# Kernel optimization log

Measured on AMD Instinct MI355X. Metric: run time of the kernel, lower is better.

## Reference

```python
import jax, jax.numpy as jnp
import numpy as np

B, C, G, K, S, P, R = 4, 256, 16, 7, 1, 3, 4
H = W = 56


def setup_inputs() -> dict:
    key = jax.random.key(0)
    k1, k2, k3 = jax.random.split(key, 3)
    x = jax.random.normal(k1, (B, C, H, W), jnp.float32)
    reduce_w = jax.random.normal(k2, (C // R, C), jnp.float32) * 0.05
    reduce_b = jnp.zeros((C // R,), jnp.float32)
    span_w = jax.random.normal(k3, (K * K * G, C // R), jnp.float32) * 0.05
    span_b = jnp.zeros((K * K * G,), jnp.float32)
    return {"x": x, "reduce_w": reduce_w, "reduce_b": reduce_b,
            "span_w": span_w, "span_b": span_b}


def reference(x, reduce_w, reduce_b, span_w, span_b):
    b, c, h_in, w_in = x.shape
    Ho = (h_in + 2 * P - K) // S + 1
    Wo = (w_in + 2 * P - K) // S + 1
    # im2col patches, channel ordering (C, kh, kw) — matches torch.nn.Unfold
    patches = jax.lax.conv_general_dilated_patches(
        x, (K, K), (S, S), [(P, P), (P, P)])  # (B, C*K*K, Ho, Wo)
    patches = patches.reshape(b, G, c // G, K * K, Ho, Wo)
    # kernel generation branch: AvgPool(s) (identity for s=1) -> 1x1 reduce -> 1x1 span
    if S > 1:
        xk = jax.lax.reduce_window(x, 0.0, jax.lax.add,
                                   (1, 1, S, S), (1, 1, S, S), 'VALID') / (S * S)
    else:
        xk = x
    h = jnp.einsum('bchw,oc->bohw', xk, reduce_w) + reduce_b[None, :, None, None]
    kern = jnp.einsum('bchw,oc->bohw', h, span_w) + span_b[None, :, None, None]
    kern = kern.reshape(b, G, 1, K * K, Ho, Wo)
    # dynamic per-pixel depthwise-style multiply-reduce over the K*K window
    out = (kern * patches).sum(axis=3)  # (B, G, C//G, Ho, Wo)
    return out.reshape(b, c, Ho, Wo)
```

## Files before the change

kernel.cpp:

```cpp
#include <hip/hip_runtime.h>
#include <hip/hip_fp16.h>
#include <stdint.h>

#define HH   56
#define WW   56
#define HWP  3136
#define CC   256
#define GG   16
#define CGR  16
#define KT   7
#define KK   49
#define RCP  32
#define TH   2
#define XROW 32
#define XPL  260

typedef _Float16 h2_t  __attribute__((ext_vector_type(2)));
typedef __fp16   fp16x2 __attribute__((ext_vector_type(2)));
typedef _Float16 v8h  __attribute__((ext_vector_type(8)));
typedef float    v4f  __attribute__((ext_vector_type(4)));
union pk32 { uint32_t u; h2_t h; __half2 hh; fp16x2 f; };
union frag { uint32_t u[4]; v8h h; };

static __device__ __forceinline__ uint32_t pkrtz(float a, float b) {
    pk32 p; p.f = __builtin_amdgcn_cvt_pkrtz(a, b); return p.u;
}

__global__ __launch_bounds__(256)
void pack_weights(const float* __restrict__ sw, const float* __restrict__ rw,
                  uint32_t* __restrict__ sw2, uint32_t* __restrict__ rw2)
{
    const int id = blockIdx.x * 256 + threadIdx.x;
    if (id < 25088) sw2[id] = pkrtz(sw[2 * id], sw[2 * id + 1]);
    else            rw2[id - 25088] = pkrtz(rw[2 * (id - 25088)], rw[2 * (id - 25088) + 1]);
}

__global__ __launch_bounds__(256)
void gemm1_mfma(const uint32_t* __restrict__ rw2, const float* __restrict__ rb,
                const float* __restrict__ x, uint32_t* __restrict__ h2)
{
    const int b = blockIdx.z, px0 = blockIdx.x * 32;
    const int t = threadIdx.x;
    const int wave = t >> 6, lane = t & 63, quad = lane >> 4, n16 = lane & 15;

    __shared__ __align__(16) uint32_t ldsB[2][8 * 128];

    const int px = t & 31;
    const int q4 = t >> 5;
    const float* xb = x + (size_t)b * CC * HWP + px0 + px;

    float r[4][8];
#pragma unroll
    for (int k = 0; k < 4; ++k)
#pragma unroll
        for (int cc = 0; cc < 8; ++cc)
            r[k][cc] = xb[(size_t)(k * 64 + q4 * 8 + cc) * HWP];

    {
        uint4 w;
        w.x = pkrtz(r[0][0], r[0][1]); w.y = pkrtz(r[0][2], r[0][3]);
        w.z = pkrtz(r[0][4], r[0][5]); w.w = pkrtz(r[0][6], r[0][7]);
        *(uint4*)&ldsB[0][q4 * 128 + px * 4] = w;
    }
    __syncthreads();

    v4f acc[2];
    acc[0] = v4f{0.f,0.f,0.f,0.f}; acc[1] = v4f{0.f,0.f,0.f,0.f};
    const uint32_t* rwm = rw2 + (size_t)(wave * 16 + n16) * 128;
#pragma unroll
    for (int k = 0; k < 4; ++k) {
        if (k < 3) {
            uint4 w;
            w.x = pkrtz(r[k+1][0], r[k+1][1]); w.y = pkrtz(r[k+1][2], r[k+1][3]);
            w.z = pkrtz(r[k+1][4], r[k+1][5]); w.w = pkrtz(r[k+1][6], r[k+1][7]);
            *(uint4*)&ldsB[(k + 1) & 1][q4 * 128 + px * 4] = w;
        }
        frag a0, a1;
        *(uint4*)a0.u = *(const uint4*)&rwm[k * 32 + quad * 4];
        *(uint4*)a1.u = *(const uint4*)&rwm[k * 32 + 16 + quad * 4];
        const uint32_t* B = ldsB[k & 1];
#pragma unroll
        for (int nt = 0; nt < 2; ++nt) {
            frag b0, b1;
            *(uint4*)b0.u = *(const uint4*)&B[quad * 128 + (nt * 16 + n16) * 4];
            *(uint4*)b1.u = *(const uint4*)&B[(4 + quad) * 128 + (nt * 16 + n16) * 4];
            acc[nt] = __builtin_amdgcn_mfma_f32_16x16x32_f16(a0.h, b0.h, acc[nt], 0, 0, 0);
            acc[nt] = __builtin_amdgcn_mfma_f32_16x16x32_f16(a1.h, b1.h, acc[nt], 0, 0, 0);
        }
        __syncthreads();
    }
    uint32_t* hb = h2 + (size_t)b * RCP * HWP + px0;
#pragma unroll
    for (int nt = 0; nt < 2; ++nt)
#pragma unroll
        for (int pr = 0; pr < 2; ++pr) {
            const int m0 = wave * 16 + quad * 4 + 2 * pr;
            hb[(size_t)(wave * 8 + quad * 2 + pr) * HWP + nt * 16 + n16] =
                pkrtz(acc[nt][2 * pr] + rb[m0], acc[nt][2 * pr + 1] + rb[m0 + 1]);
        }
}

__global__ __launch_bounds__(256, 4)
void invol_fused(const float* __restrict__ x, const uint32_t* __restrict__ h2,
                 const uint32_t* __restrict__ sw2, const float* __restrict__ sb,
                 float* __restrict__ out)
{
    const int h0 = blockIdx.x * TH, g = blockIdx.y, b = blockIdx.z;

    __shared__ __align__(16) uint32_t sXh[16 * XPL];
    __shared__ __align__(16) uint32_t U[8 * 448];

    const int t = threadIdx.x;
    const int wave = t >> 6, lane = t & 63, quad = lane >> 4, n16 = lane & 15;

    const int mt0 = wave * 16 + n16;
    const int mtap = mt0 > 48 ? 48 : mt0;
    const uint32_t* swr = sw2 + ((size_t)g * KK + mtap) * RCP + quad * 4;
    frag a0, a1;
    *(uint4*)a0.u = *(const uint4*)swr;
    *(uint4*)a1.u = *(const uint4*)(swr + 16);

    float bvv[4];
#pragma unroll
    for (int reg = 0; reg < 4; ++reg) {
        const int tp = wave * 16 + quad * 4 + reg;
        bvv[reg] = (tp < KK) ? sb[g * KK + tp] : 0.f;
    }

    {
        const uint32_t* hb = h2 + (size_t)b * RCP * HWP + h0 * WW;
#pragma unroll
        for (int k = 0; k < 4; ++k) {
            const int i = t + 256 * k;
            if (i < 896) {
                const int px = i % 112, q4 = i / 112;
                uint4 w;
                w.x = hb[(size_t)(q4 * 4 + 0) * HWP + px];
                w.y = hb[(size_t)(q4 * 4 + 1) * HWP + px];
                w.z = hb[(size_t)(q4 * 4 + 2) * HWP + px];
                w.w = hb[(size_t)(q4 * 4 + 3) * HWP + px];
                *(uint4*)&U[q4 * 448 + px * 4] = w;
            }
        }
    }

    {
        const int ch = t >> 4, rr = (t >> 1) & 7, side = t & 1;
        uint2 z; z.x = 0; z.y = 0;
        *(uint2*)&sXh[ch * XPL + rr * XROW + (side ? 30 : 0)] = z;
    }

    {
        const float* xb = x + (size_t)(b * CC + g * CGR) * HWP;
#pragma unroll
        for (int k = 0; k < 7; ++k) {
            const int i = t + 256 * k;
            const int w4 = i % 14, rr = (i / 14) % 8, ch = i / 112;
            const int hh = h0 - 3 + rr;
            float4 v = make_float4(0.f, 0.f, 0.f, 0.f);
            if (hh >= 0 && hh < HH)
                v = *(const float4*)&xb[(size_t)ch * HWP + hh * WW + 4 * w4];
            uint2 p; p.x = pkrtz(v.x, v.y); p.y = pkrtz(v.z, v.w);
            *(uint2*)&sXh[ch * XPL + rr * XROW + 2 + 2 * w4] = p;
        }
    }
    __syncthreads();

    v4f acc[7];
#pragma unroll
    for (int nt = 0; nt < 7; ++nt) acc[nt] = v4f{0.f,0.f,0.f,0.f};
#pragma unroll
    for (int nt = 0; nt < 7; ++nt) {
        const int pxm = (nt * 16 + n16) * 4;
        frag b0, b1;
        *(uint4*)b0.u = *(const uint4*)&U[quad * 448 + pxm];
        *(uint4*)b1.u = *(const uint4*)&U[(4 + quad) * 448 + pxm];
        acc[nt] = __builtin_amdgcn_mfma_f32_16x16x32_f16(a0.h, b0.h, acc[nt], 0, 0, 0);
        acc[nt] = __builtin_amdgcn_mfma_f32_16x16x32_f16(a1.h, b1.h, acc[nt], 0, 0, 0);
    }
    __syncthreads();

    {
        _Float16* sK = (_Float16*)U;
#pragma unroll
        for (int nt = 0; nt < 7; ++nt) {
            const int px = nt * 16 + n16;
#pragma unroll
            for (int reg = 0; reg < 4; ++reg) {
                const int tp = wave * 16 + quad * 4 + reg;
                if (tp < KK) sK[tp * 112 + px] = (_Float16)(acc[nt][reg] + bvv[reg]);
            }
        }
    }
    __syncthreads();

    if (t < 224) {
        const int ch = t & 15, q = t >> 4, r = q & 1, wq = q >> 1;
        const uint32_t* xpl = &sXh[ch * XPL + 4 * wq];
        float o0=0,o1=0,o2=0,o3=0,o4=0,o5=0,o6=0,o7=0;
#pragma unroll
        for (int kh = 0; kh < KT; ++kh) {
            const int rr = r + kh;
            uint32_t E[8];
            *(uint4*)&E[0] = *(const uint4*)&xpl[rr * XROW];
            *(uint4*)&E[4] = *(const uint4*)&xpl[rr * XROW + 4];
            uint32_t O[7];
#pragma unroll
            for (int j = 0; j < 7; ++j) O[j] = __builtin_amdgcn_alignbit(E[j + 1], E[j], 16);
            pk32 va0, va1, va2, va3;
            va0.u = va1.u = va2.u = va3.u = 0;
            const uint32_t* kq = &U[(kh * KT) * 56 + r * 28 + 4 * wq];
#pragma unroll
            for (int kw = 0; kw < KT; ++kw) {
                const uint4 kk = *(const uint4*)&kq[kw * 56];
                pk32 k0, k1, k2, k3; k0.u = kk.x; k1.u = kk.y; k2.u = kk.z; k3.u = kk.w;
                pk32 s0, s1, s2, s3;
                if (kw & 1) {
                    const int e = (kw + 1) >> 1;
                    s0.u = E[e]; s1.u = E[e + 1]; s2.u = E[e + 2]; s3.u = E[e + 3];
                } else {
                    const int oI = kw >> 1;
                    s0.u = O[oI]; s1.u = O[oI + 1]; s2.u = O[oI + 2]; s3.u = O[oI + 3];
                }
                va0.hh = __hfma2(k0.hh, s0.hh, va0.hh);
                va1.hh = __hfma2(k1.hh, s1.hh, va1.hh);
                va2.hh = __hfma2(k2.hh, s2.hh, va2.hh);
                va3.hh = __hfma2(k3.hh, s3.hh, va3.hh);
            }
            const float2 f0 = __half22float2(va0.hh); o0 += f0.x; o1 += f0.y;
            const float2 f1 = __half22float2(va1.hh); o2 += f1.x; o3 += f1.y;
            const float2 f2 = __half22float2(va2.hh); o4 += f2.x; o5 += f2.y;
            const float2 f3 = __half22float2(va3.hh); o6 += f3.x; o7 += f3.y;
        }
        float* op = out + (size_t)(b * CC + g * CGR + ch) * HWP + (h0 + r) * WW + 8 * wq;
        *(float4*)&op[0] = make_float4(o0, o1, o2, o3);
        *(float4*)&op[4] = make_float4(o4, o5, o6, o7);
    }
}

extern "C" void kernel_launch(void* const* d_in, const int* in_sizes, int n_in,
                              void* d_out, int out_size, void* d_ws, size_t ws_size,
                              hipStream_t stream)
{
    const float* x  = (const float*)d_in[0];
    const float* rw = (const float*)d_in[1];
    const float* rb = (const float*)d_in[2];
    const float* sw = (const float*)d_in[3];
    const float* sb = (const float*)d_in[4];
    float* out  = (float*)d_out;

    uint32_t* h2  = (uint32_t*)d_ws;
    uint32_t* sw2 = h2 + 4 * RCP * HWP;
    uint32_t* rw2 = sw2 + 25088;

    pack_weights<<<dim3(130, 1, 1), 256, 0, stream>>>(sw, rw, sw2, rw2);
    gemm1_mfma<<<dim3(HWP / 32, 1, 4), 256, 0, stream>>>(rw2, rb, x, h2);
    invol_fused<<<dim3(HH / TH, GG, 4), 256, 0, stream>>>(x, h2, sw2, sb, out);
}
```

Measured before the change: 96.14 us.

## Drop weight-pack kernel, enlarge involution row tile, two channels per thread

Removes the separate pack_weights launch; both GEMM kernels now read fp32 weights and convert them to fp16 fragments inline. The first GEMM halves its pixel tile to 16 so it launches more blocks. The involution kernel doubles its row tile to 4 rows (more MFMA tiles, larger LDS, fewer halo rows per output) and each thread now handles two channels so the kernel-weight LDS loads are reused. In exchange, LDS use and registers per block go up and occupancy drops to 3 blocks per unit, and the involution grid shrinks by half.

```diff
diff --git a/kernel.cpp b/kernel.cpp
--- a/kernel.cpp
+++ b/kernel.cpp
@@ -11,14 +11,16 @@
 #define KT   7
 #define KK   49
 #define RCP  32
-#define TH   2
-#define XROW 32
-#define XPL  260
-
-typedef _Float16 h2_t  __attribute__((ext_vector_type(2)));
+#define TH   4
+#define NPX  (TH * WW)
+#define XROW 36
+#define XPL  364
+#define BQ4  (NPX * 4)
+
+typedef _Float16 h2_t   __attribute__((ext_vector_type(2)));
 typedef __fp16   fp16x2 __attribute__((ext_vector_type(2)));
-typedef _Float16 v8h  __attribute__((ext_vector_type(8)));
-typedef float    v4f  __attribute__((ext_vector_type(4)));
+typedef _Float16 v8h    __attribute__((ext_vector_type(8)));
+typedef float    v4f    __attribute__((ext_vector_type(4)));
 union pk32 { uint32_t u; h2_t h; __half2 hh; fp16x2 f; };
 union frag { uint32_t u[4]; v8h h; };
 
@@ -26,99 +28,86 @@
     pk32 p; p.f = __builtin_amdgcn_cvt_pkrtz(a, b); return p.u;
 }
 
+static __device__ __forceinline__ frag pack_afrag(const float* rowp, int quad) {
+    frag a;
+    const float4 p0 = *(const float4*)&rowp[quad * 8];
+    const float4 p1 = *(const float4*)&rowp[quad * 8 + 4];
+    a.u[0] = pkrtz(p0.x, p0.y); a.u[1] = pkrtz(p0.z, p0.w);
+    a.u[2] = pkrtz(p1.x, p1.y); a.u[3] = pkrtz(p1.z, p1.w);
+    return a;
+}
+
 __global__ __launch_bounds__(256)
-void pack_weights(const float* __restrict__ sw, const float* __restrict__ rw,
-                  uint32_t* __restrict__ sw2, uint32_t* __restrict__ rw2)
-{
-    const int id = blockIdx.x * 256 + threadIdx.x;
-    if (id < 25088) sw2[id] = pkrtz(sw[2 * id], sw[2 * id + 1]);
-    else            rw2[id - 25088] = pkrtz(rw[2 * (id - 25088)], rw[2 * (id - 25088) + 1]);
-}
-
-__global__ __launch_bounds__(256)
-void gemm1_mfma(const uint32_t* __restrict__ rw2, const float* __restrict__ rb,
+void gemm1_mfma(const float* __restrict__ rw, const float* __restrict__ rb,
                 const float* __restrict__ x, uint32_t* __restrict__ h2)
 {
-    const int b = blockIdx.z, px0 = blockIdx.x * 32;
+    const int b = blockIdx.z, px0 = blockIdx.x * 16;
     const int t = threadIdx.x;
     const int wave = t >> 6, lane = t & 63, quad = lane >> 4, n16 = lane & 15;
 
-    __shared__ __align__(16) uint32_t ldsB[2][8 * 128];
-
-    const int px = t & 31;
-    const int q4 = t >> 5;
+    __shared__ __align__(16) uint32_t ldsB[2][512];
+
+    const int px = t & 15;
+    const int cp = t >> 4;
     const float* xb = x + (size_t)b * CC * HWP + px0 + px;
 
-    float r[4][8];
-#pragma unroll
-    for (int k = 0; k < 4; ++k)
-#pragma unroll
-        for (int cc = 0; cc < 8; ++cc)
-            r[k][cc] = xb[(size_t)(k * 64 + q4 * 8 + cc) * HWP];
-
-    {
-        uint4 w;
-        w.x = pkrtz(r[0][0], r[0][1]); w.y = pkrtz(r[0][2], r[0][3]);
-        w.z = pkrtz(r[0][4], r[0][5]); w.w = pkrtz(r[0][6], r[0][7]);
-        *(uint4*)&ldsB[0][q4 * 128 + px * 4] = w;
-    }
-    __syncthreads();
-
-    v4f acc[2];
-    acc[0] = v4f{0.f,0.f,0.f,0.f}; acc[1] = v4f{0.f,0.f,0.f,0.f};
-    const uint32_t* rwm = rw2 + (size_t)(wave * 16 + n16) * 128;
+    float ra[4][4];
+#pragma unroll
+    for (int k = 0; k < 4; ++k) {
+        ra[k][0] = xb[(size_t)(k * 64 + 2 * cp) * HWP];
+        ra[k][1] = xb[(size_t)(k * 64 + 2 * cp + 1) * HWP];
+        ra[k][2] = xb[(size_t)(k * 64 + 2 * cp + 32) * HWP];
+        ra[k][3] = xb[(size_t)(k * 64 + 2 * cp + 33) * HWP];
+    }
+    const int q4a = cp >> 2, jja = cp & 3;
+    ldsB[0][q4a * 64 + px * 4 + jja]       = pkrtz(ra[0][0], ra[0][1]);
+    ldsB[0][(q4a + 4) * 64 + px * 4 + jja] = pkrtz(ra[0][2], ra[0][3]);
+    __syncthreads();
+
+    const float* rwr = rw + (size_t)(wave * 16 + n16) * CC;
+    v4f acc = v4f{0.f, 0.f, 0.f, 0.f};
 #pragma unroll
     for (int k = 0; k < 4; ++k) {
         if (k < 3) {
-            uint4 w;
-            w.x = pkrtz(r[k+1][0], r[k+1][1]); w.y = pkrtz(r[k+1][2], r[k+1][3]);
-            w.z = pkrtz(r[k+1][4], r[k+1][5]); w.w = pkrtz(r[k+1][6], r[k+1][7]);
-            *(uint4*)&ldsB[(k + 1) & 1][q4 * 128 + px * 4] = w;
-        }
-        frag a0, a1;
-        *(uint4*)a0.u = *(const uint4*)&rwm[k * 32 + quad * 4];
-        *(uint4*)a1.u = *(const uint4*)&rwm[k * 32 + 16 + quad * 4];
-        const uint32_t* B = ldsB[k & 1];
-#pragma unroll
-        for (int nt = 0; nt < 2; ++nt) {
-            frag b0, b1;
-            *(uint4*)b0.u = *(const uint4*)&B[quad * 128 + (nt * 16 + n16) * 4];
-            *(uint4*)b1.u = *(const uint4*)&B[(4 + quad) * 128 + (nt * 16 + n16) * 4];
-            acc[nt] = __builtin_amdgcn_mfma_f32_16x16x32_f16(a0.h, b0.h, acc[nt], 0, 0, 0);
-            acc[nt] = __builtin_amdgcn_mfma_f32_16x16x32_f16(a1.h, b1.h, acc[nt], 0, 0, 0);
-        }
-        __syncthreads();
+            ldsB[(k + 1) & 1][q4a * 64 + px * 4 + jja]       = pkrtz(ra[k+1][0], ra[k+1][1]);
+            ldsB[(k + 1) & 1][(q4a + 4) * 64 + px * 4 + jja] = pkrtz(ra[k+1][2], ra[k+1][3]);
+        }
+        const frag a0 = pack_afrag(rwr + k * 64, quad);
+        const frag a1 = pack_afrag(rwr + k * 64 + 32, quad);
+        frag b0, b1;
+        *(uint4*)b0.u = *(const uint4*)&ldsB[k & 1][quad * 64 + n16 * 4];
+        *(uint4*)b1.u = *(const uint4*)&ldsB[k & 1][(4 + quad) * 64 + n16 * 4];
+        acc = __builtin_amdgcn_mfma_f32_16x16x32_f16(a0.h, b0.h, acc, 0, 0, 0);
+        acc = __builtin_amdgcn_mfma_f32_16x16x32_f16(a1.h, b1.h, acc, 0, 0, 0);
+        if (k < 3) __syncthreads();
     }
     uint32_t* hb = h2 + (size_t)b * RCP * HWP + px0;
 #pragma unroll
-    for (int nt = 0; nt < 2; ++nt)
-#pragma unroll
-        for (int pr = 0; pr < 2; ++pr) {
-            const int m0 = wave * 16 + quad * 4 + 2 * pr;
-            hb[(size_t)(wave * 8 + quad * 2 + pr) * HWP + nt * 16 + n16] =
-                pkrtz(acc[nt][2 * pr] + rb[m0], acc[nt][2 * pr + 1] + rb[m0 + 1]);
-        }
-}
-
-__global__ __launch_bounds__(256, 4)
+    for (int pr = 0; pr < 2; ++pr) {
+        const int m0 = wave * 16 + quad * 4 + 2 * pr;
+        hb[(size_t)(wave * 8 + quad * 2 + pr) * HWP + n16] =
+            pkrtz(acc[2 * pr] + rb[m0], acc[2 * pr + 1] + rb[m0 + 1]);
+    }
+}
+
+__global__ __launch_bounds__(256, 3)
 void invol_fused(const float* __restrict__ x, const uint32_t* __restrict__ h2,
-                 const uint32_t* __restrict__ sw2, const float* __restrict__ sb,
+                 const float* __restrict__ sw, const float* __restrict__ sb,
                  float* __restrict__ out)
 {
     const int h0 = blockIdx.x * TH, g = blockIdx.y, b = blockIdx.z;
 
     __shared__ __align__(16) uint32_t sXh[16 * XPL];
-    __shared__ __align__(16) uint32_t U[8 * 448];
+    __shared__ __align__(16) uint32_t U[8 * BQ4];
 
     const int t = threadIdx.x;
     const int wave = t >> 6, lane = t & 63, quad = lane >> 4, n16 = lane & 15;
 
     const int mt0 = wave * 16 + n16;
     const int mtap = mt0 > 48 ? 48 : mt0;
-    const uint32_t* swr = sw2 + ((size_t)g * KK + mtap) * RCP + quad * 4;
-    frag a0, a1;
-    *(uint4*)a0.u = *(const uint4*)swr;
-    *(uint4*)a1.u = *(const uint4*)(swr + 16);
+    const float* swr = sw + (size_t)(g * KK + mtap) * 64;
+    const frag a0 = pack_afrag(swr, quad);
+    const frag a1 = pack_afrag(swr + 32, quad);
 
     float bvv[4];
 #pragma unroll
@@ -130,51 +119,55 @@
     {
         const uint32_t* hb = h2 + (size_t)b * RCP * HWP + h0 * WW;
 #pragma unroll
-        for (int k = 0; k < 4; ++k) {
+        for (int k = 0; k < 7; ++k) {
             const int i = t + 256 * k;
-            if (i < 896) {
-                const int px = i % 112, q4 = i / 112;
-                uint4 w;
-                w.x = hb[(size_t)(q4 * 4 + 0) * HWP + px];
-                w.y = hb[(size_t)(q4 * 4 + 1) * HWP + px];
-                w.z = hb[(size_t)(q4 * 4 + 2) * HWP + px];
-                w.w = hb[(size_t)(q4 * 4 + 3) * HWP + px];
-                *(uint4*)&U[q4 * 448 + px * 4] = w;
-            }
-        }
-    }
-
-    {
-        const int ch = t >> 4, rr = (t >> 1) & 7, side = t & 1;
-        uint2 z; z.x = 0; z.y = 0;
-        *(uint2*)&sXh[ch * XPL + rr * XROW + (side ? 30 : 0)] = z;
+            const int px = i % NPX, q4 = i / NPX;
+            uint4 w;
+            w.x = hb[(size_t)(q4 * 4 + 0) * HWP + px];
+            w.y = hb[(size_t)(q4 * 4 + 1) * HWP + px];
+            w.z = hb[(size_t)(q4 * 4 + 2) * HWP + px];
+            w.w = hb[(size_t)(q4 * 4 + 3) * HWP + px];
+            *(uint4*)&U[q4 * BQ4 + px * 4] = w;
+        }
+    }
+
+#pragma unroll
+    for (int k = 0; k < 2; ++k) {
+        const int i = t + 256 * k;
+        if (i < 320) {
+            const int ch = i / 20, rem = i % 20, rr = rem >> 1, side = rem & 1;
+            uint2 z; z.x = 0; z.y = 0;
+            *(uint2*)&sXh[ch * XPL + rr * XROW + (side ? 30 : 0)] = z;
+        }
     }
 
     {
         const float* xb = x + (size_t)(b * CC + g * CGR) * HWP;
 #pragma unroll
-        for (int k = 0; k < 7; ++k) {
+        for (int k = 0; k < 9; ++k) {
             const int i = t + 256 * k;
-            const int w4 = i % 14, rr = (i / 14) % 8, ch = i / 112;
-            const int hh = h0 - 3 + rr;
-            float4 v = make_float4(0.f, 0.f, 0.f, 0.f);
-            if (hh >= 0 && hh < HH)
-                v = *(const float4*)&xb[(size_t)ch * HWP + hh * WW + 4 * w4];
-            uint2 p; p.x = pkrtz(v.x, v.y); p.y = pkrtz(v.z, v.w);
-            *(uint2*)&sXh[ch * XPL + rr * XROW + 2 + 2 * w4] = p;
-        }
-    }
-    __syncthreads();
-
-    v4f acc[7];
-#pragma unroll
-    for (int nt = 0; nt < 7; ++nt) acc[nt] = v4f{0.f,0.f,0.f,0.f};
-#pragma unroll
-    for (int nt = 0; nt < 7; ++nt) {
+            if (i < 2240) {
+                const int w4 = i % 14, rr = (i / 14) % 10, ch = i / 140;
+                const int hh = h0 - 3 + rr;
+                float4 v = make_float4(0.f, 0.f, 0.f, 0.f);
+                if (hh >= 0 && hh < HH)
+                    v = *(const float4*)&xb[(size_t)ch * HWP + hh * WW + 4 * w4];
+                uint2 p; p.x = pkrtz(v.x, v.y); p.y = pkrtz(v.z, v.w);
+                *(uint2*)&sXh[ch * XPL + rr * XROW + 2 + 2 * w4] = p;
+            }
+        }
+    }
+    __syncthreads();
+
+    v4f acc[14];
+#pragma unroll
+    for (int nt = 0; nt < 14; ++nt) acc[nt] = v4f{0.f, 0.f, 0.f, 0.f};
+#pragma unroll
+    for (int nt = 0; nt < 14; ++nt) {
         const int pxm = (nt * 16 + n16) * 4;
         frag b0, b1;
-        *(uint4*)b0.u = *(const uint4*)&U[quad * 448 + pxm];
-        *(uint4*)b1.u = *(const uint4*)&U[(4 + quad) * 448 + pxm];
+        *(uint4*)b0.u = *(const uint4*)&U[quad * BQ4 + pxm];
+        *(uint4*)b1.u = *(const uint4*)&U[(4 + quad) * BQ4 + pxm];
         acc[nt] = __builtin_amdgcn_mfma_f32_16x16x32_f16(a0.h, b0.h, acc[nt], 0, 0, 0);
         acc[nt] = __builtin_amdgcn_mfma_f32_16x16x32_f16(a1.h, b1.h, acc[nt], 0, 0, 0);
     }
@@ -183,58 +176,91 @@
     {
         _Float16* sK = (_Float16*)U;
 #pragma unroll
-        for (int nt = 0; nt < 7; ++nt) {
+        for (int nt = 0; nt < 14; ++nt) {
             const int px = nt * 16 + n16;
 #pragma unroll
             for (int reg = 0; reg < 4; ++reg) {
                 const int tp = wave * 16 + quad * 4 + reg;
-                if (tp < KK) sK[tp * 112 + px] = (_Float16)(acc[nt][reg] + bvv[reg]);
+                if (tp < KK) sK[tp * NPX + px] = (_Float16)(acc[nt][reg] + bvv[reg]);
             }
         }
     }
     __syncthreads();
 
     if (t < 224) {
-        const int ch = t & 15, q = t >> 4, r = q & 1, wq = q >> 1;
-        const uint32_t* xpl = &sXh[ch * XPL + 4 * wq];
-        float o0=0,o1=0,o2=0,o3=0,o4=0,o5=0,o6=0,o7=0;
+        const int chq = t & 7, q = t >> 3;
+        const int r = q / 7, wq = q % 7;
+        const int ch0 = 2 * chq;
+        const uint32_t* xp0 = &sXh[ch0 * XPL + 4 * wq];
+        const uint32_t* xp1 = &sXh[(ch0 + 1) * XPL + 4 * wq];
+        float oa[2][8];
+#pragma unroll
+        for (int c = 0; c < 2; ++c)
+#pragma unroll
+            for (int j = 0; j < 8; ++j) oa[c][j] = 0.f;
+
 #pragma unroll
         for (int kh = 0; kh < KT; ++kh) {
             const int rr = r + kh;
-            uint32_t E[8];
-            *(uint4*)&E[0] = *(const uint4*)&xpl[rr * XROW];
-            *(uint4*)&E[4] = *(const uint4*)&xpl[rr * XROW + 4];
-            uint32_t O[7];
-#pragma unroll
-            for (int j = 0; j < 7; ++j) O[j] = __builtin_amdgcn_alignbit(E[j + 1], E[j], 16);
-            pk32 va0, va1, va2, va3;
-            va0.u = va1.u = va2.u = va3.u = 0;
-            const uint32_t* kq = &U[(kh * KT) * 56 + r * 28 + 4 * wq];
+            uint32_t E0[8], E1[8], O0[7], O1[7];
+            *(uint4*)&E0[0] = *(const uint4*)&xp0[rr * XROW];
+            *(uint4*)&E0[4] = *(const uint4*)&xp0[rr * XROW + 4];
+            *(uint4*)&E1[0] = *(const uint4*)&xp1[rr * XROW];
+            *(uint4*)&E1[4] = *(const uint4*)&xp1[rr * XROW + 4];
+#pragma unroll
+            for (int j = 0; j < 7; ++j) {
+                O0[j] = __builtin_amdgcn_alignbit(E0[j + 1], E0[j], 16);
+                O1[j] = __builtin_amdgcn_alignbit(E1[j + 1], E1[j], 16);
+            }
+            pk32 va[2][4];
+#pragma unroll
+            for (int c = 0; c < 2; ++c)
+#pragma unroll
+                for (int j = 0; j < 4; ++j) va[c][j].u = 0;
+
+            const uint32_t* kq = &U[(kh * KT) * (NPX / 2) + r * 28 + 4 * wq];
 #pragma unroll
             for (int kw = 0; kw < KT; ++kw) {
-                const uint4 kk = *(const uint4*)&kq[kw * 56];
+                const uint4 kk = *(const uint4*)&kq[kw * (NPX / 2)];
                 pk32 k0, k1, k2, k3; k0.u = kk.x; k1.u = kk.y; k2.u = kk.z; k3.u = kk.w;
-                pk32 s0, s1, s2, s3;
+                uint32_t s0, s1, s2, s3, u0, u1, u2, u3;
                 if (kw & 1) {
                     const int e = (kw + 1) >> 1;
-                    s0.u = E[e]; s1.u = E[e + 1]; s2.u = E[e + 2]; s3.u = E[e + 3];
+                    s0 = E0[e]; s1 = E0[e + 1]; s2 = E0[e + 2]; s3 = E0[e + 3];
+                    u0 = E1[e]; u1 = E1[e + 1]; u2 = E1[e + 2]; u3 = E1[e + 3];
                 } else {
                     const int oI = kw >> 1;
-                    s0.u = O[oI]; s1.u = O[oI + 1]; s2.u = O[oI + 2]; s3.u = O[oI + 3];
+                    s0 = O0[oI]; s1 = O0[oI + 1]; s2 = O0[oI + 2]; s3 = O0[oI + 3];
+                    u0 = O1[oI]; u1 = O1[oI + 1]; u2 = O1[oI + 2]; u3 = O1[oI + 3];
                 }
-                va0.hh = __hfma2(k0.hh, s0.hh, va0.hh);
-                va1.hh = __hfma2(k1.hh, s1.hh, va1.hh);
-                va2.hh = __hfma2(k2.hh, s2.hh, va2.hh);
-                va3.hh = __hfma2(k3.hh, s3.hh, va3.hh);
-            }
-            const float2 f0 = __half22float2(va0.hh); o0 += f0.x; o1 += f0.y;
-            const float2 f1 = __half22float2(va1.hh); o2 += f1.x; o3 += f1.y;
-            const float2 f2 = __half22float2(va2.hh); o4 += f2.x; o5 += f2.y;
-            const float2 f3 = __half22float2(va3.hh); o6 += f3.x; o7 += f3.y;
-        }
-        float* op = out + (size_t)(b * CC + g * CGR + ch) * HWP + (h0 + r) * WW + 8 * wq;
-        *(float4*)&op[0] = make_float4(o0, o1, o2, o3);
-        *(float4*)&op[4] = make_float4(o4, o5, o6, o7);
+                pk32 t0, t1, t2, t3;
+                t0.u = s0; t1.u = s1; t2.u = s2; t3.u = s3;
+                va[0][0].hh = __hfma2(k0.hh, t0.hh, va[0][0].hh);
+                va[0][1].hh = __hfma2(k1.hh, t1.hh, va[0][1].hh);
+                va[0][2].hh = __hfma2(k2.hh, t2.hh, va[0][2].hh);
+                va[0][3].hh = __hfma2(k3.hh, t3.hh, va[0][3].hh);
+                t0.u = u0; t1.u = u1; t2.u = u2; t3.u = u3;
+                va[1][0].hh = __hfma2(k0.hh, t0.hh, va[1][0].hh);
+                va[1][1].hh = __hfma2(k1.hh, t1.hh, va[1][1].hh);
+                va[1][2].hh = __hfma2(k2.hh, t2.hh, va[1][2].hh);
+                va[1][3].hh = __hfma2(k3.hh, t3.hh, va[1][3].hh);
+            }
+#pragma unroll
+            for (int c = 0; c < 2; ++c)
+#pragma unroll
+                for (int j = 0; j < 4; ++j) {
+                    const float2 f = __half22float2(va[c][j].hh);
+                    oa[c][2 * j]     += f.x;
+                    oa[c][2 * j + 1] += f.y;
+                }
+        }
+#pragma unroll
+        for (int c = 0; c < 2; ++c) {
+            float* op = out + (size_t)(b * CC + g * CGR + ch0 + c) * HWP
+                            + (h0 + r) * WW + 8 * wq;
+            *(float4*)&op[0] = make_float4(oa[c][0], oa[c][1], oa[c][2], oa[c][3]);
+            *(float4*)&op[4] = make_float4(oa[c][4], oa[c][5], oa[c][6], oa[c][7]);
+        }
     }
 }
 
@@ -249,11 +275,8 @@
     const float* sb = (const float*)d_in[4];
     float* out  = (float*)d_out;
 
-    uint32_t* h2  = (uint32_t*)d_ws;
-    uint32_t* sw2 = h2 + 4 * RCP * HWP;
-    uint32_t* rw2 = sw2 + 25088;
-
-    pack_weights<<<dim3(130, 1, 1), 256, 0, stream>>>(sw, rw, sw2, rw2);
-    gemm1_mfma<<<dim3(HWP / 32, 1, 4), 256, 0, stream>>>(rw2, rb, x, h2);
-    invol_fused<<<dim3(HH / TH, GG, 4), 256, 0, stream>>>(x, h2, sw2, sb, out);
-}
+    uint32_t* h2 = (uint32_t*)d_ws;
+
+    gemm1_mfma<<<dim3(HWP / 16, 1, 4), 256, 0, stream>>>(rw, rb, x, h2);
+    invol_fused<<<dim3(HH / TH, GG, 4), 256, 0, stream>>>(x, h2, sw, sb, out);
+}
```

Result: slower. 103.3 us (+7.4%).

## Fuse weight packing into consumer kernels and compute two channels per thread

Applied to the files above, without the earlier changes.

Removes the separate pack_weights launch: gemm1 and invol_fused now read fp32 weights directly and convert them to fp16 MFMA fragments in registers. The involution reduction stage now has 112 threads, each handling two channels, so every kernel-weight LDS load feeds twice as many FMAs. This saves one kernel launch and the round trip through the workspace. In exchange it adds redundant per-block conversion work, raises register pressure, and halves the thread parallelism of the reduction stage.

```diff
diff --git a/kernel.cpp b/kernel.cpp
--- a/kernel.cpp
+++ b/kernel.cpp
@@ -15,10 +15,10 @@
 #define XROW 32
 #define XPL  260
 
-typedef _Float16 h2_t  __attribute__((ext_vector_type(2)));
+typedef _Float16 h2_t   __attribute__((ext_vector_type(2)));
 typedef __fp16   fp16x2 __attribute__((ext_vector_type(2)));
-typedef _Float16 v8h  __attribute__((ext_vector_type(8)));
-typedef float    v4f  __attribute__((ext_vector_type(4)));
+typedef _Float16 v8h    __attribute__((ext_vector_type(8)));
+typedef float    v4f    __attribute__((ext_vector_type(4)));
 union pk32 { uint32_t u; h2_t h; __half2 hh; fp16x2 f; };
 union frag { uint32_t u[4]; v8h h; };
 
@@ -26,17 +26,17 @@
     pk32 p; p.f = __builtin_amdgcn_cvt_pkrtz(a, b); return p.u;
 }
 
+static __device__ __forceinline__ frag pack_afrag(const float* rowp, int quad) {
+    frag a;
+    const float4 p0 = *(const float4*)&rowp[quad * 8];
+    const float4 p1 = *(const float4*)&rowp[quad * 8 + 4];
+    a.u[0] = pkrtz(p0.x, p0.y); a.u[1] = pkrtz(p0.z, p0.w);
+    a.u[2] = pkrtz(p1.x, p1.y); a.u[3] = pkrtz(p1.z, p1.w);
+    return a;
+}
+
 __global__ __launch_bounds__(256)
-void pack_weights(const float* __restrict__ sw, const float* __restrict__ rw,
-                  uint32_t* __restrict__ sw2, uint32_t* __restrict__ rw2)
-{
-    const int id = blockIdx.x * 256 + threadIdx.x;
-    if (id < 25088) sw2[id] = pkrtz(sw[2 * id], sw[2 * id + 1]);
-    else            rw2[id - 25088] = pkrtz(rw[2 * (id - 25088)], rw[2 * (id - 25088) + 1]);
-}
-
-__global__ __launch_bounds__(256)
-void gemm1_mfma(const uint32_t* __restrict__ rw2, const float* __restrict__ rb,
+void gemm1_mfma(const float* __restrict__ rw, const float* __restrict__ rb,
                 const float* __restrict__ x, uint32_t* __restrict__ h2)
 {
     const int b = blockIdx.z, px0 = blockIdx.x * 32;
@@ -56,6 +56,14 @@
         for (int cc = 0; cc < 8; ++cc)
             r[k][cc] = xb[(size_t)(k * 64 + q4 * 8 + cc) * HWP];
 
+    const float* rwr = rw + (size_t)(wave * 16 + n16) * CC;
+    frag af0[4], af1[4];
+#pragma unroll
+    for (int k = 0; k < 4; ++k) {
+        af0[k] = pack_afrag(rwr + k * 64, quad);
+        af1[k] = pack_afrag(rwr + k * 64 + 32, quad);
+    }
+
     {
         uint4 w;
         w.x = pkrtz(r[0][0], r[0][1]); w.y = pkrtz(r[0][2], r[0][3]);
@@ -66,7 +74,6 @@
 
     v4f acc[2];
     acc[0] = v4f{0.f,0.f,0.f,0.f}; acc[1] = v4f{0.f,0.f,0.f,0.f};
-    const uint32_t* rwm = rw2 + (size_t)(wave * 16 + n16) * 128;
 #pragma unroll
     for (int k = 0; k < 4; ++k) {
         if (k < 3) {
@@ -75,17 +82,14 @@
             w.z = pkrtz(r[k+1][4], r[k+1][5]); w.w = pkrtz(r[k+1][6], r[k+1][7]);
             *(uint4*)&ldsB[(k + 1) & 1][q4 * 128 + px * 4] = w;
         }
-        frag a0, a1;
-        *(uint4*)a0.u = *(const uint4*)&rwm[k * 32 + quad * 4];
-        *(uint4*)a1.u = *(const uint4*)&rwm[k * 32 + 16 + quad * 4];
         const uint32_t* B = ldsB[k & 1];
 #pragma unroll
         for (int nt = 0; nt < 2; ++nt) {
             frag b0, b1;
             *(uint4*)b0.u = *(const uint4*)&B[quad * 128 + (nt * 16 + n16) * 4];
             *(uint4*)b1.u = *(const uint4*)&B[(4 + quad) * 128 + (nt * 16 + n16) * 4];
-            acc[nt] = __builtin_amdgcn_mfma_f32_16x16x32_f16(a0.h, b0.h, acc[nt], 0, 0, 0);
-            acc[nt] = __builtin_amdgcn_mfma_f32_16x16x32_f16(a1.h, b1.h, acc[nt], 0, 0, 0);
+            acc[nt] = __builtin_amdgcn_mfma_f32_16x16x32_f16(af0[k].h, b0.h, acc[nt], 0, 0, 0);
+            acc[nt] = __builtin_amdgcn_mfma_f32_16x16x32_f16(af1[k].h, b1.h, acc[nt], 0, 0, 0);
         }
         __syncthreads();
     }
@@ -102,7 +106,7 @@
 
 __global__ __launch_bounds__(256, 4)
 void invol_fused(const float* __restrict__ x, const uint32_t* __restrict__ h2,
-                 const uint32_t* __restrict__ sw2, const float* __restrict__ sb,
+                 const float* __restrict__ sw, const float* __restrict__ sb,
                  float* __restrict__ out)
 {
     const int h0 = blockIdx.x * TH, g = blockIdx.y, b = blockIdx.z;
@@ -115,10 +119,9 @@
 
     const int mt0 = wave * 16 + n16;
     const int mtap = mt0 > 48 ? 48 : mt0;
-    const uint32_t* swr = sw2 + ((size_t)g * KK + mtap) * RCP + quad * 4;
-    frag a0, a1;
-    *(uint4*)a0.u = *(const uint4*)swr;
-    *(uint4*)a1.u = *(const uint4*)(swr + 16);
+    const float* swr = sw + (size_t)(g * KK + mtap) * 64;
+    const frag a0 = pack_afrag(swr, quad);
+    const frag a1 = pack_afrag(swr + 32, quad);
 
     float bvv[4];
 #pragma unroll
@@ -194,21 +197,37 @@
     }
     __syncthreads();
 
-    if (t < 224) {
-        const int ch = t & 15, q = t >> 4, r = q & 1, wq = q >> 1;
-        const uint32_t* xpl = &sXh[ch * XPL + 4 * wq];
-        float o0=0,o1=0,o2=0,o3=0,o4=0,o5=0,o6=0,o7=0;
+    if (t < 112) {
+        const int chp = t & 7, q = t >> 3;
+        const int r = q & 1, wq = q >> 1;
+        const int ch0 = 2 * chp;
+        const uint32_t* xp0 = &sXh[ch0 * XPL + 4 * wq];
+        const uint32_t* xp1 = &sXh[(ch0 + 1) * XPL + 4 * wq];
+        float oa[2][8];
+#pragma unroll
+        for (int c = 0; c < 2; ++c)
+#pragma unroll
+            for (int j = 0; j < 8; ++j) oa[c][j] = 0.f;
+
 #pragma unroll
         for (int kh = 0; kh < KT; ++kh) {
             const int rr = r + kh;
-            uint32_t E[8];
-            *(uint4*)&E[0] = *(const uint4*)&xpl[rr * XROW];
-            *(uint4*)&E[4] = *(const uint4*)&xpl[rr * XROW + 4];
-            uint32_t O[7];
-#pragma unroll
-            for (int j = 0; j < 7; ++j) O[j] = __builtin_amdgcn_alignbit(E[j + 1], E[j], 16);
-            pk32 va0, va1, va2, va3;
-            va0.u = va1.u = va2.u = va3.u = 0;
+            uint32_t E0[8], E1[8], O0[7], O1[7];
+            *(uint4*)&E0[0] = *(const uint4*)&xp0[rr * XROW];
+            *(uint4*)&E0[4] = *(const uint4*)&xp0[rr * XROW + 4];
+            *(uint4*)&E1[0] = *(const uint4*)&xp1[rr * XROW];
+            *(uint4*)&E1[4] = *(const uint4*)&xp1[rr * XROW + 4];
+#pragma unroll
+            for (int j = 0; j < 7; ++j) {
+                O0[j] = __builtin_amdgcn_alignbit(E0[j + 1], E0[j], 16);
+                O1[j] = __builtin_amdgcn_alignbit(E1[j + 1], E1[j], 16);
+            }
+            pk32 va[2][4];
+#pragma unroll
+            for (int c = 0; c < 2; ++c)
+#pragma unroll
+                for (int j = 0; j < 4; ++j) va[c][j].u = 0;
+
             const uint32_t* kq = &U[(kh * KT) * 56 + r * 28 + 4 * wq];
 #pragma unroll
             for (int kw = 0; kw < KT; ++kw) {
@@ -217,24 +236,43 @@
                 pk32 s0, s1, s2, s3;
                 if (kw & 1) {
                     const int e = (kw + 1) >> 1;
-                    s0.u = E[e]; s1.u = E[e + 1]; s2.u = E[e + 2]; s3.u = E[e + 3];
+                    s0.u = E0[e]; s1.u = E0[e + 1]; s2.u = E0[e + 2]; s3.u = E0[e + 3];
                 } else {
                     const int oI = kw >> 1;
-                    s0.u = O[oI]; s1.u = O[oI + 1]; s2.u = O[oI + 2]; s3.u = O[oI + 3];
+                    s0.u = O0[oI]; s1.u = O0[oI + 1]; s2.u = O0[oI + 2]; s3.u = O0[oI + 3];
                 }
-                va0.hh = __hfma2(k0.hh, s0.hh, va0.hh);
-                va1.hh = __hfma2(k1.hh, s1.hh, va1.hh);
-                va2.hh = __hfma2(k2.hh, s2.hh, va2.hh);
-                va3.hh = __hfma2(k3.hh, s3.hh, va3.hh);
-            }
-            const float2 f0 = __half22float2(va0.hh); o0 += f0.x; o1 += f0.y;
-            const float2 f1 = __half22float2(va1.hh); o2 += f1.x; o3 += f1.y;
-            const float2 f2 = __half22float2(va2.hh); o4 += f2.x; o5 += f2.y;
-            const float2 f3 = __half22float2(va3.hh); o6 += f3.x; o7 += f3.y;
-        }
-        float* op = out + (size_t)(b * CC + g * CGR + ch) * HWP + (h0 + r) * WW + 8 * wq;
-        *(float4*)&op[0] = make_float4(o0, o1, o2, o3);
-        *(float4*)&op[4] = make_float4(o4, o5, o6, o7);
+                va[0][0].hh = __hfma2(k0.hh, s0.hh, va[0][0].hh);
+                va[0][1].hh = __hfma2(k1.hh, s1.hh, va[0][1].hh);
+                va[0][2].hh = __hfma2(k2.hh, s2.hh, va[0][2].hh);
+                va[0][3].hh = __hfma2(k3.hh, s3.hh, va[0][3].hh);
+                if (kw & 1) {
+                    const int e = (kw + 1) >> 1;
+                    s0.u = E1[e]; s1.u = E1[e + 1]; s2.u = E1[e + 2]; s3.u = E1[e + 3];
+                } else {
+                    const int oI = kw >> 1;
+                    s0.u = O1[oI]; s1.u = O1[oI + 1]; s2.u = O1[oI + 2]; s3.u = O1[oI + 3];
+                }
+                va[1][0].hh = __hfma2(k0.hh, s0.hh, va[1][0].hh);
+                va[1][1].hh = __hfma2(k1.hh, s1.hh, va[1][1].hh);
+                va[1][2].hh = __hfma2(k2.hh, s2.hh, va[1][2].hh);
+                va[1][3].hh = __hfma2(k3.hh, s3.hh, va[1][3].hh);
+            }
+#pragma unroll
+            for (int c = 0; c < 2; ++c)
+#pragma unroll
+                for (int j = 0; j < 4; ++j) {
+                    const float2 f = __half22float2(va[c][j].hh);
+                    oa[c][2 * j]     += f.x;
+                    oa[c][2 * j + 1] += f.y;
+                }
+        }
+#pragma unroll
+        for (int c = 0; c < 2; ++c) {
+            float* op = out + (size_t)(b * CC + g * CGR + ch0 + c) * HWP
+                            + (h0 + r) * WW + 8 * wq;
+            *(float4*)&op[0] = make_float4(oa[c][0], oa[c][1], oa[c][2], oa[c][3]);
+            *(float4*)&op[4] = make_float4(oa[c][4], oa[c][5], oa[c][6], oa[c][7]);
+        }
     }
 }
 
@@ -249,11 +287,8 @@
     const float* sb = (const float*)d_in[4];
     float* out  = (float*)d_out;
 
-    uint32_t* h2  = (uint32_t*)d_ws;
-    uint32_t* sw2 = h2 + 4 * RCP * HWP;
-    uint32_t* rw2 = sw2 + 25088;
-
-    pack_weights<<<dim3(130, 1, 1), 256, 0, stream>>>(sw, rw, sw2, rw2);
-    gemm1_mfma<<<dim3(HWP / 32, 1, 4), 256, 0, stream>>>(rw2, rb, x, h2);
-    invol_fused<<<dim3(HH / TH, GG, 4), 256, 0, stream>>>(x, h2, sw2, sb, out);
-}
+    uint32_t* h2 = (uint32_t*)d_ws;
+
+    gemm1_mfma<<<dim3(HWP / 32, 1, 4), 256, 0, stream>>>(rw, rb, x, h2);
+    invol_fused<<<dim3(HH / TH, GG, 4), 256, 0, stream>>>(x, h2, sw, sb, out);
+}
```

Result: no change. 97.63 us (+1.5%).

## Fold reduce and span 1x1 convs into one weight, fuse GEMM into involution

Applied to the files above, without the earlier changes.

Precomputes a combined weight span_w·reduce_w (784x256) and bias in a small fold kernel, removing the separate gemm1 kernel and the intermediate h buffer. Each involution block now computes its kernel taps directly from x over all 256 channels with MFMA, double-buffering x chunks in LDS. This drops a launch and the h round trip through memory, but each of the 16 group blocks per row pair re-reads the full 256-channel x slice. The GEMM work therefore grows about 8x (256-deep per tap instead of 32-deep), and the launch bound is lowered to 3 blocks per CU.

```diff
diff --git a/kernel.cpp b/kernel.cpp
--- a/kernel.cpp
+++ b/kernel.cpp
@@ -10,15 +10,14 @@
 #define CGR  16
 #define KT   7
 #define KK   49
-#define RCP  32
 #define TH   2
 #define XROW 32
 #define XPL  260
 
-typedef _Float16 h2_t  __attribute__((ext_vector_type(2)));
+typedef _Float16 h2_t   __attribute__((ext_vector_type(2)));
 typedef __fp16   fp16x2 __attribute__((ext_vector_type(2)));
-typedef _Float16 v8h  __attribute__((ext_vector_type(8)));
-typedef float    v4f  __attribute__((ext_vector_type(4)));
+typedef _Float16 v8h    __attribute__((ext_vector_type(8)));
+typedef float    v4f    __attribute__((ext_vector_type(4)));
 union pk32 { uint32_t u; h2_t h; __half2 hh; fp16x2 f; };
 union frag { uint32_t u[4]; v8h h; };
 
@@ -27,120 +26,70 @@
 }
 
 __global__ __launch_bounds__(256)
-void pack_weights(const float* __restrict__ sw, const float* __restrict__ rw,
-                  uint32_t* __restrict__ sw2, uint32_t* __restrict__ rw2)
+void fold(const float* __restrict__ sw, const float* __restrict__ rw,
+          const float* __restrict__ rb, const float* __restrict__ sb,
+          uint32_t* __restrict__ wc2, float* __restrict__ bc)
 {
-    const int id = blockIdx.x * 256 + threadIdx.x;
-    if (id < 25088) sw2[id] = pkrtz(sw[2 * id], sw[2 * id + 1]);
-    else            rw2[id - 25088] = pkrtz(rw[2 * (id - 25088)], rw[2 * (id - 25088) + 1]);
-}
-
-__global__ __launch_bounds__(256)
-void gemm1_mfma(const uint32_t* __restrict__ rw2, const float* __restrict__ rb,
-                const float* __restrict__ x, uint32_t* __restrict__ h2)
+    const int t = threadIdx.x;
+    const int row = blockIdx.x * 2 + (t >> 7);
+    const int pp  = t & 127;
+    const float* swr = sw + (size_t)row * 64;
+    float a0 = 0.f, a1 = 0.f;
+#pragma unroll
+    for (int c = 0; c < 64; ++c) {
+        const float s = swr[c];
+        const float2 rv = *(const float2*)&rw[(size_t)c * CC + 2 * pp];
+        a0 += s * rv.x; a1 += s * rv.y;
+    }
+    wc2[(size_t)row * 128 + pp] = pkrtz(a0, a1);
+    if (pp == 0) {
+        float bacc = 0.f;
+        for (int c = 0; c < 64; ++c) bacc += swr[c] * rb[c];
+        bc[row] = bacc + sb[row];
+    }
+}
+
+__global__ __launch_bounds__(256, 3)
+void invol_fused(const float* __restrict__ x, const uint32_t* __restrict__ wc2,
+                 const float* __restrict__ bc, float* __restrict__ out)
 {
-    const int b = blockIdx.z, px0 = blockIdx.x * 32;
+    const int h0 = blockIdx.x * TH, g = blockIdx.y, b = blockIdx.z;
+
+    __shared__ __align__(16) uint32_t sXh[16 * XPL];
+    __shared__ __align__(16) uint32_t ldsB[2][3584];
+
     const int t = threadIdx.x;
     const int wave = t >> 6, lane = t & 63, quad = lane >> 4, n16 = lane & 15;
 
-    __shared__ __align__(16) uint32_t ldsB[2][8 * 128];
-
-    const int px = t & 31;
-    const int q4 = t >> 5;
-    const float* xb = x + (size_t)b * CC * HWP + px0 + px;
-
-    float r[4][8];
-#pragma unroll
-    for (int k = 0; k < 4; ++k)
-#pragma unroll
-        for (int cc = 0; cc < 8; ++cc)
-            r[k][cc] = xb[(size_t)(k * 64 + q4 * 8 + cc) * HWP];
-
-    {
-        uint4 w;
-        w.x = pkrtz(r[0][0], r[0][1]); w.y = pkrtz(r[0][2], r[0][3]);
-        w.z = pkrtz(r[0][4], r[0][5]); w.w = pkrtz(r[0][6], r[0][7]);
-        *(uint4*)&ldsB[0][q4 * 128 + px * 4] = w;
-    }
-    __syncthreads();
-
-    v4f acc[2];
-    acc[0] = v4f{0.f,0.f,0.f,0.f}; acc[1] = v4f{0.f,0.f,0.f,0.f};
-    const uint32_t* rwm = rw2 + (size_t)(wave * 16 + n16) * 128;
-#pragma unroll
-    for (int k = 0; k < 4; ++k) {
-        if (k < 3) {
-            uint4 w;
-            w.x = pkrtz(r[k+1][0], r[k+1][1]); w.y = pkrtz(r[k+1][2], r[k+1][3]);
-            w.z = pkrtz(r[k+1][4], r[k+1][5]); w.w = pkrtz(r[k+1][6], r[k+1][7]);
-            *(uint4*)&ldsB[(k + 1) & 1][q4 * 128 + px * 4] = w;
-        }
-        frag a0, a1;
-        *(uint4*)a0.u = *(const uint4*)&rwm[k * 32 + quad * 4];
-        *(uint4*)a1.u = *(const uint4*)&rwm[k * 32 + 16 + quad * 4];
-        const uint32_t* B = ldsB[k & 1];
-#pragma unroll
-        for (int nt = 0; nt < 2; ++nt) {
-            frag b0, b1;
-            *(uint4*)b0.u = *(const uint4*)&B[quad * 128 + (nt * 16 + n16) * 4];
-            *(uint4*)b1.u = *(const uint4*)&B[(4 + quad) * 128 + (nt * 16 + n16) * 4];
-            acc[nt] = __builtin_amdgcn_mfma_f32_16x16x32_f16(a0.h, b0.h, acc[nt], 0, 0, 0);
-            acc[nt] = __builtin_amdgcn_mfma_f32_16x16x32_f16(a1.h, b1.h, acc[nt], 0, 0, 0);
-        }
-        __syncthreads();
-    }
-    uint32_t* hb = h2 + (size_t)b * RCP * HWP + px0;
-#pragma unroll
-    for (int nt = 0; nt < 2; ++nt)
-#pragma unroll
-        for (int pr = 0; pr < 2; ++pr) {
-            const int m0 = wave * 16 + quad * 4 + 2 * pr;
-            hb[(size_t)(wave * 8 + quad * 2 + pr) * HWP + nt * 16 + n16] =
-                pkrtz(acc[nt][2 * pr] + rb[m0], acc[nt][2 * pr + 1] + rb[m0 + 1]);
-        }
-}
-
-__global__ __launch_bounds__(256, 4)
-void invol_fused(const float* __restrict__ x, const uint32_t* __restrict__ h2,
-                 const uint32_t* __restrict__ sw2, const float* __restrict__ sb,
-                 float* __restrict__ out)
-{
-    const int h0 = blockIdx.x * TH, g = blockIdx.y, b = blockIdx.z;
-
-    __shared__ __align__(16) uint32_t sXh[16 * XPL];
-    __shared__ __align__(16) uint32_t U[8 * 448];
-
-    const int t = threadIdx.x;
-    const int wave = t >> 6, lane = t & 63, quad = lane >> 4, n16 = lane & 15;
+    const float* xb = x + (size_t)b * CC * HWP + h0 * WW;
 
     const int mt0 = wave * 16 + n16;
     const int mtap = mt0 > 48 ? 48 : mt0;
-    const uint32_t* swr = sw2 + ((size_t)g * KK + mtap) * RCP + quad * 4;
-    frag a0, a1;
-    *(uint4*)a0.u = *(const uint4*)swr;
-    *(uint4*)a1.u = *(const uint4*)(swr + 16);
+    const uint32_t* wr = wc2 + (size_t)(g * KK + mtap) * 128;
+    frag af[8];
+#pragma unroll
+    for (int kc = 0; kc < 8; ++kc)
+        *(uint4*)af[kc].u = *(const uint4*)&wr[kc * 16 + quad * 4];
 
     float bvv[4];
 #pragma unroll
     for (int reg = 0; reg < 4; ++reg) {
         const int tp = wave * 16 + quad * 4 + reg;
-        bvv[reg] = (tp < KK) ? sb[g * KK + tp] : 0.f;
-    }
-
-    {
-        const uint32_t* hb = h2 + (size_t)b * RCP * HWP + h0 * WW;
-#pragma unroll
-        for (int k = 0; k < 4; ++k) {
-            const int i = t + 256 * k;
-            if (i < 896) {
-                const int px = i % 112, q4 = i / 112;
-                uint4 w;
-                w.x = hb[(size_t)(q4 * 4 + 0) * HWP + px];
-                w.y = hb[(size_t)(q4 * 4 + 1) * HWP + px];
-                w.z = hb[(size_t)(q4 * 4 + 2) * HWP + px];
-                w.w = hb[(size_t)(q4 * 4 + 3) * HWP + px];
-                *(uint4*)&U[q4 * 448 + px * 4] = w;
-            }
+        bvv[reg] = (tp < KK) ? bc[g * KK + tp] : 0.f;
+    }
+
+#pragma unroll
+    for (int k = 0; k < 4; ++k) {
+        const int s = t + 256 * k;
+        if (s < 896) {
+            const int q4 = s / 112, px = s % 112;
+            const float* xc = xb + (size_t)(q4 * 8) * HWP + px;
+            uint4 w;
+            w.x = pkrtz(xc[0],          xc[(size_t)1 * HWP]);
+            w.y = pkrtz(xc[(size_t)2 * HWP], xc[(size_t)3 * HWP]);
+            w.z = pkrtz(xc[(size_t)4 * HWP], xc[(size_t)5 * HWP]);
+            w.w = pkrtz(xc[(size_t)6 * HWP], xc[(size_t)7 * HWP]);
+            *(uint4*)&ldsB[0][(q4 * 112 + px) * 4] = w;
         }
     }
 
@@ -149,9 +98,8 @@
         uint2 z; z.x = 0; z.y = 0;
         *(uint2*)&sXh[ch * XPL + rr * XROW + (side ? 30 : 0)] = z;
     }
-
     {
-        const float* xb = x + (size_t)(b * CC + g * CGR) * HWP;
+        const float* xg = x + (size_t)(b * CC + g * CGR) * HWP;
 #pragma unroll
         for (int k = 0; k < 7; ++k) {
             const int i = t + 256 * k;
@@ -159,7 +107,7 @@
             const int hh = h0 - 3 + rr;
             float4 v = make_float4(0.f, 0.f, 0.f, 0.f);
             if (hh >= 0 && hh < HH)
-                v = *(const float4*)&xb[(size_t)ch * HWP + hh * WW + 4 * w4];
+                v = *(const float4*)&xg[(size_t)ch * HWP + hh * WW + 4 * w4];
             uint2 p; p.x = pkrtz(v.x, v.y); p.y = pkrtz(v.z, v.w);
             *(uint2*)&sXh[ch * XPL + rr * XROW + 2 + 2 * w4] = p;
         }
@@ -168,20 +116,41 @@
 
     v4f acc[7];
 #pragma unroll
-    for (int nt = 0; nt < 7; ++nt) acc[nt] = v4f{0.f,0.f,0.f,0.f};
-#pragma unroll
-    for (int nt = 0; nt < 7; ++nt) {
-        const int pxm = (nt * 16 + n16) * 4;
-        frag b0, b1;
-        *(uint4*)b0.u = *(const uint4*)&U[quad * 448 + pxm];
-        *(uint4*)b1.u = *(const uint4*)&U[(4 + quad) * 448 + pxm];
-        acc[nt] = __builtin_amdgcn_mfma_f32_16x16x32_f16(a0.h, b0.h, acc[nt], 0, 0, 0);
-        acc[nt] = __builtin_amdgcn_mfma_f32_16x16x32_f16(a1.h, b1.h, acc[nt], 0, 0, 0);
-    }
-    __syncthreads();
+    for (int nt = 0; nt < 7; ++nt) acc[nt] = v4f{0.f, 0.f, 0.f, 0.f};
+#pragma unroll
+    for (int kc = 0; kc < 4; ++kc) {
+        if (kc < 3) {
+            uint32_t* buf = ldsB[(kc + 1) & 1];
+#pragma unroll
+            for (int k = 0; k < 4; ++k) {
+                const int s = t + 256 * k;
+                if (s < 896) {
+                    const int q4 = s / 112, px = s % 112;
+                    const float* xc = xb + (size_t)((kc + 1) * 64 + q4 * 8) * HWP + px;
+                    uint4 w;
+                    w.x = pkrtz(xc[0],          xc[(size_t)1 * HWP]);
+                    w.y = pkrtz(xc[(size_t)2 * HWP], xc[(size_t)3 * HWP]);
+                    w.z = pkrtz(xc[(size_t)4 * HWP], xc[(size_t)5 * HWP]);
+                    w.w = pkrtz(xc[(size_t)6 * HWP], xc[(size_t)7 * HWP]);
+                    *(uint4*)&buf[(q4 * 112 + px) * 4] = w;
+                }
+            }
+        }
+        const uint32_t* B = ldsB[kc & 1];
+#pragma unroll
+        for (int nt = 0; nt < 7; ++nt) {
+            const int pxm = (nt * 16 + n16) * 4;
+            frag b0, b1;
+            *(uint4*)b0.u = *(const uint4*)&B[quad * 448 + pxm];
+            *(uint4*)b1.u = *(const uint4*)&B[(4 + quad) * 448 + pxm];
+            acc[nt] = __builtin_amdgcn_mfma_f32_16x16x32_f16(af[2 * kc].h,     b0.h, acc[nt], 0, 0, 0);
+            acc[nt] = __builtin_amdgcn_mfma_f32_16x16x32_f16(af[2 * kc + 1].h, b1.h, acc[nt], 0, 0, 0);
+        }
+        __syncthreads();
+    }
 
     {
-        _Float16* sK = (_Float16*)U;
+        _Float16* sK = (_Float16*)ldsB[0];
 #pragma unroll
         for (int nt = 0; nt < 7; ++nt) {
             const int px = nt * 16 + n16;
@@ -197,6 +166,7 @@
     if (t < 224) {
         const int ch = t & 15, q = t >> 4, r = q & 1, wq = q >> 1;
         const uint32_t* xpl = &sXh[ch * XPL + 4 * wq];
+        const uint32_t* U = ldsB[0];
         float o0=0,o1=0,o2=0,o3=0,o4=0,o5=0,o6=0,o7=0;
 #pragma unroll
         for (int kh = 0; kh < KT; ++kh) {
@@ -249,11 +219,9 @@
     const float* sb = (const float*)d_in[4];
     float* out  = (float*)d_out;
 
-    uint32_t* h2  = (uint32_t*)d_ws;
-    uint32_t* sw2 = h2 + 4 * RCP * HWP;
-    uint32_t* rw2 = sw2 + 25088;
-
-    pack_weights<<<dim3(130, 1, 1), 256, 0, stream>>>(sw, rw, sw2, rw2);
-    gemm1_mfma<<<dim3(HWP / 32, 1, 4), 256, 0, stream>>>(rw2, rb, x, h2);
-    invol_fused<<<dim3(HH / TH, GG, 4), 256, 0, stream>>>(x, h2, sw2, sb, out);
-}
+    uint32_t* wc2 = (uint32_t*)d_ws;
+    float*    bcb = (float*)(wc2 + 784 * 128);
+
+    fold<<<dim3(392, 1, 1), 256, 0, stream>>>(sw, rw, rb, sb, wc2, bcb);
+    invol_fused<<<dim3(HH / TH, GG, 4), 256, 0, stream>>>(x, wc2, bcb, out);
+}
```

Result: slower. 119.9 us (+24.8%).
